# Performance work log

Hardware: AMD Instinct MI355X
Metric: run time of the kernel (lower is better)

The kernel has to match this reference:

```python
import jax, jax.numpy as jnp
import numpy as np

B, N, S, NS = 16, 4096, 512, 32
RADIUS = 0.4
EPS = 1e-5
CHANS = [6, 64, 64, 128]


def setup_inputs() -> dict:
    key = jax.random.key(0)
    ks = jax.random.split(key, 8)
    inp = {
        "xyz": jax.random.normal(ks[0], (B, 3, N), jnp.float32),
        "points": jax.random.normal(ks[1], (B, 3, N), jnp.float32),
    }
    for i in range(3):
        cin, cout = CHANS[i], CHANS[i + 1]
        inp[f"w{i}"] = jax.random.normal(ks[2 + i], (cout, cin), jnp.float32) * (1.0 / np.sqrt(cin))
        inp[f"b{i}"] = jnp.zeros((cout,), jnp.float32)
        inp[f"g{i}"] = jnp.ones((cout,), jnp.float32)
        inp[f"beta{i}"] = jnp.zeros((cout,), jnp.float32)
    return inp


def _fps(xyz):
    # xyz: [B, N, 3] -> indices [B, S] (deterministic start at index 0)
    n = xyz.shape[1]

    def step(carry, _):
        dist, far = carry
        centroid = jnp.take_along_axis(xyz, far[:, None, None], axis=1)  # [B,1,3]
        d = jnp.sum((xyz - centroid) ** 2, -1)                           # [B,N]
        dist = jnp.minimum(dist, d)
        nxt = jnp.argmax(dist, axis=-1).astype(jnp.int32)
        return (dist, nxt), far

    init = (jnp.full((xyz.shape[0], n), 1e10, xyz.dtype), jnp.zeros((xyz.shape[0],), jnp.int32))
    _, idx = jax.lax.scan(step, init, None, length=S)
    return idx.T  # [B, S]


def _query_ball(xyz, new_xyz):
    # xyz: [B,N,3], new_xyz: [B,S,3] -> group indices [B,S,NS]
    n = xyz.shape[1]
    sqr = (jnp.sum(new_xyz ** 2, -1)[:, :, None]
           + jnp.sum(xyz ** 2, -1)[:, None, :]
           - 2.0 * jnp.einsum('bsc,bnc->bsn', new_xyz, xyz))  # [B,S,N]
    grp = jnp.where(sqr <= RADIUS ** 2, jnp.arange(n, dtype=jnp.int32)[None, None, :], n)
    grp = jnp.sort(grp, axis=-1)[:, :, :NS]
    first = grp[:, :, :1]
    return jnp.where(grp == n, first, grp)


_gather = jax.vmap(lambda p, i: p[i])  # p:[N,C], i:[S,NS] -> [S,NS,C]


def _forward(xyz, points, params):
    xyz_t = jnp.transpose(xyz, (0, 2, 1))      # [B,N,3]
    pts_t = jnp.transpose(points, (0, 2, 1))   # [B,N,D]
    fps_idx = _fps(xyz_t)                      # [B,S]
    new_xyz = jnp.take_along_axis(xyz_t, fps_idx[:, :, None], axis=1)  # [B,S,3]
    grp = _query_ball(xyz_t, new_xyz)          # [B,S,NS]
    grouped_xyz = _gather(xyz_t, grp) - new_xyz[:, :, None, :]         # [B,S,NS,3]
    grouped_pts = _gather(pts_t, grp)          # [B,S,NS,D]
    feat = jnp.concatenate([grouped_xyz, grouped_pts], axis=-1)        # [B,S,NS,3+D]
    x = jnp.transpose(feat, (0, 3, 2, 1))      # [B,C,NS,S]
    for (w, b, g, beta) in params:
        x = jnp.einsum('oc,bcns->bons', w, x) + b[None, :, None, None]
        mean = jnp.mean(x, axis=(0, 2, 3), keepdims=True)
        var = jnp.mean((x - mean) ** 2, axis=(0, 2, 3), keepdims=True)
        x = (x - mean) * jax.lax.rsqrt(var + EPS)
        x = jax.nn.relu(x * g[None, :, None, None] + beta[None, :, None, None])
    new_points = jnp.max(x, axis=2)            # [B, C_out, S]
    return jnp.transpose(new_xyz, (0, 2, 1)), new_points


def reference(xyz, points, w0, b0, g0, beta0, w1, b1, g1, beta1, w2, b2, g2, beta2):
    params = [(w0, b0, g0, beta0), (w1, b1, g1, beta1), (w2, b2, g2, beta2)]
    return _forward(xyz, points, params)
```

## Files before the change

kernel.cpp:

```cpp
#include <hip/hip_runtime.h>
#include <math.h>

#define BB 16
#define NN 4096
#define SS 512
#define KK 32
#define NPIX (BB*SS*KK)
#define NGRP (BB*SS)

static constexpr float R2F  = (float)0.16000000000000003;
static constexpr float EPSF = 1e-5f;

constexpr size_t OFF_NXYZ = 0;
constexpr size_t OFF_GRP  = 98304;
constexpr size_t OFF_P1   = 98304 + 1048576;
constexpr size_t OFF_P2   = OFF_P1 + 32768;
constexpr size_t OFF_P3   = OFF_P2 + 32768;
constexpr size_t OFF_MR1  = OFF_P3 + 65536;
constexpr size_t OFF_MR2  = OFF_MR1 + 512;
constexpr size_t OFF_MR3  = OFF_MR2 + 512;
constexpr size_t OFF_Z3   = 2*1024*1024;
constexpr size_t Z3SZ     = (size_t)NPIX*128*4;
constexpr size_t OFF_Z2   = OFF_Z3 + Z3SZ;
constexpr size_t Z2SZ     = (size_t)NPIX*64*4;
constexpr size_t NEED_Z3  = OFF_Z3 + Z3SZ;
constexpr size_t NEED_Z2  = OFF_Z2 + Z2SZ;

#define DPP_FMAX(v, ctrl) { int _t = __builtin_amdgcn_update_dpp(              \
      __float_as_int(v), __float_as_int(v), ctrl, 0xf, 0xf, false);            \
      v = fmaxf(v, __int_as_float(_t)); }
#define DPP_UMIN(v, ctrl) { unsigned _t = (unsigned)__builtin_amdgcn_update_dpp( \
      (int)(v), (int)(v), ctrl, 0xf, 0xf, false);                              \
      v = (v < _t ? v : _t); }

__global__ __launch_bounds__(512) void fps_kernel(const float* __restrict__ xyz,
        float* __restrict__ out0, float* __restrict__ nxyz){
  const int b = blockIdx.x;
  const float* xb = xyz + (size_t)b*3*NN;
  __shared__ float4 pt4[NN];
  __shared__ __align__(16) unsigned long long skey[2][8];
  __shared__ int hist[SS];
  const int t = threadIdx.x;
  const int lane = t & 63, wv = t >> 6;
  float rx[8], ry[8], rz[8], rd[8];
#pragma unroll
  for (int j=0;j<8;j++){
    int i = t + 512*j;
    float x = xb[i], y = xb[NN+i], z = xb[2*NN+i];
    rx[j]=x; ry[j]=y; rz[j]=z;
    pt4[i] = make_float4(x,y,z,0.0f);
    rd[j]=1e10f;
  }
  __syncthreads();
  int far = 0;
  for (int s=0;s<SS;s++){
    const int buf = s & 1;
    float4 c = pt4[far];
    if (t==0) hist[s] = far;
    float bv = -1.0f;
#pragma unroll
    for (int j=0;j<8;j++){
      float dx=__fsub_rn(rx[j],c.x), dy=__fsub_rn(ry[j],c.y), dz=__fsub_rn(rz[j],c.z);
      float d2=__fadd_rn(__fadd_rn(__fmul_rn(dx,dx),__fmul_rn(dy,dy)),__fmul_rn(dz,dz));
      float nd=fminf(rd[j],d2);
      rd[j]=nd;
      bv = fmaxf(bv, nd);
    }
    DPP_FMAX(bv,0x111); DPP_FMAX(bv,0x112); DPP_FMAX(bv,0x114);
    DPP_FMAX(bv,0x118); DPP_FMAX(bv,0x142); DPP_FMAX(bv,0x143);
    const float vmax = __int_as_float(__builtin_amdgcn_readlane(__float_as_int(bv), 63));
    unsigned cand = 0xFFFFFFFFu;
#pragma unroll
    for (int j=7;j>=0;j--) if (rd[j]==vmax) cand = (unsigned)(t+512*j);
    DPP_UMIN(cand,0x111); DPP_UMIN(cand,0x112); DPP_UMIN(cand,0x114);
    DPP_UMIN(cand,0x118); DPP_UMIN(cand,0x142); DPP_UMIN(cand,0x143);
    if (lane==63){
      skey[buf][wv] = ((unsigned long long)(unsigned)__float_as_int(vmax) << 32)
                    | (unsigned)(~cand);
    }
    __syncthreads();
    unsigned long long k0=skey[buf][0], k1=skey[buf][1], k2=skey[buf][2], k3=skey[buf][3];
    unsigned long long k4=skey[buf][4], k5=skey[buf][5], k6=skey[buf][6], k7=skey[buf][7];
    unsigned long long m01=(k0>k1)?k0:k1, m23=(k2>k3)?k2:k3;
    unsigned long long m45=(k4>k5)?k4:k5, m67=(k6>k7)?k6:k7;
    unsigned long long mA=(m01>m23)?m01:m23, mB=(m45>m67)?m45:m67;
    unsigned long long m =(mA>mB)?mA:mB;
    far = (int)(~(unsigned)(m & 0xFFFFFFFFull));
  }
  __syncthreads();
  {
    int idx = hist[t];
    float4 c = pt4[idx];
    int gid = b*SS + t;
    nxyz[gid*3+0]=c.x; nxyz[gid*3+1]=c.y; nxyz[gid*3+2]=c.z;
    out0[(b*3+0)*SS+t]=c.x; out0[(b*3+1)*SS+t]=c.y; out0[(b*3+2)*SS+t]=c.z;
  }
}

__global__ __launch_bounds__(256) void ball_kernel(const float* __restrict__ xyz,
        const float* __restrict__ nxyz, int* __restrict__ grp){
  const int gw   = (blockIdx.x*256 + threadIdx.x) >> 6;
  const int lane = threadIdx.x & 63;
  if (gw >= NGRP) return;
  const int b = gw / SS;
  const float* xb = xyz + (size_t)b*3*NN;
  const float nx=nxyz[gw*3+0], ny=nxyz[gw*3+1], nz=nxyz[gw*3+2];
  const float sn = __fadd_rn(__fadd_rn(__fmul_rn(nx,nx),__fmul_rn(ny,ny)),__fmul_rn(nz,nz));
  int cnt=0, first=-1;
  int* g = grp + (size_t)gw*KK;
  for (int c=0;c<NN/64 && cnt<KK;c++){
    int i=c*64+lane;
    float x=xb[i], y=xb[NN+i], z=xb[2*NN+i];
    float sxx=__fadd_rn(__fadd_rn(__fmul_rn(x,x),__fmul_rn(y,y)),__fmul_rn(z,z));
    float dot=__fadd_rn(__fadd_rn(__fmul_rn(nx,x),__fmul_rn(ny,y)),__fmul_rn(nz,z));
    float sqr=__fsub_rn(__fadd_rn(sn,sxx),__fmul_rn(2.0f,dot));
    bool m = (sqr <= R2F);
    unsigned long long mask = __ballot(m);
    if (m){
      int pos = cnt + __popcll(mask & ((1ull<<lane)-1ull));
      if (pos < KK) g[pos] = i;
    }
    if (first<0 && mask) first = c*64 + (__ffsll((long long)mask) - 1);
    cnt += __popcll(mask);
  }
  if (cnt < KK && lane >= cnt && lane < KK) g[lane] = first;
}

__global__ void finalize_kernel(const double* __restrict__ part, float* __restrict__ mr, int C){
  int o = threadIdx.x;
  if (o < C){
    double s1=0.0, s2=0.0;
    for (int k=0;k<32;k++){ s1 += part[o*32+k]; s2 += part[(C+o)*32+k]; }
    const double n = (double)NPIX;
    double mean = s1/n;
    double var  = s2/n - mean*mean;
    mr[2*o]   = (float)mean;
    mr[2*o+1] = (float)(1.0/sqrt(var + (double)EPSF));
  }
}

constexpr int XIN = 0;
constexpr int W0F = 408;
constexpr int B0F = 792;
constexpr int W1F = 856;
constexpr int B1F = 4952;
constexpr int XBF = 5016;
constexpr int SRF = 9368;
constexpr int W2F = 9624;
constexpr int B2F = 17816;
constexpr int SM_SMALL = 9624;
constexpr int SM_BIG   = 17944;

template<int STAGE, bool STZ3, bool Z2IO>
__global__ __launch_bounds__(256,2) void mlp_kernel(
    const float* __restrict__ xyz, const float* __restrict__ pts,
    const float* __restrict__ nxyz, const int* __restrict__ grp,
    const float* __restrict__ w0, const float* __restrict__ b0,
    const float* __restrict__ mr1, const float* __restrict__ g0, const float* __restrict__ be0,
    const float* __restrict__ w1, const float* __restrict__ b1,
    const float* __restrict__ mr2, const float* __restrict__ g1, const float* __restrict__ be1,
    const float* __restrict__ w2, const float* __restrict__ b2,
    const float* __restrict__ mr3, const float* __restrict__ g2, const float* __restrict__ be2,
    double* __restrict__ part, float* __restrict__ out1,
    float* __restrict__ z2w, float* __restrict__ z3w)
{
  __shared__ float sm[(STAGE>=3)? SM_BIG : SM_SMALL];
  const int t   = threadIdx.x;
  const int blk = blockIdx.x;
  const int tx  = t & 15, ty = t >> 4;
  const int p0  = blk*64;
  const int slot = blk & 31;
  constexpr bool SKIP12 = (STAGE==3 && Z2IO);

  sm[SRF + t] = 0.0f;

  if constexpr (!SKIP12){
    for (int i=t;i<384;i+=256){ int o=i/6, c=i-o*6; sm[W0F + c*64 + o] = w0[i]; }
    if (t<64) sm[B0F+t] = b0[t];
    if constexpr (STAGE>=2){
      for (int i=t;i<4096;i+=256){ int o=i&63, c=i>>6; sm[W1F + c*64 + o] = w1[o*64+c]; }
      if (t<64) sm[B1F+t] = b1[t];
    }
    for (int i=t;i<384;i+=256){
      int c=i>>6, px=i&63, p=p0+px, gid=p>>5, bb=p>>14;
      int idx = grp[p];
      float v;
      if (c<3) v = __fsub_rn(xyz[(size_t)bb*3*NN + c*NN + idx], nxyz[gid*3+c]);
      else     v = pts[(size_t)bb*3*NN + (c-3)*NN + idx];
      sm[XIN + c*68 + px] = v;
    }
  }
  if constexpr (STAGE>=3){
    for (int i=t;i<8192;i+=256){ int o=i&127, c=i>>7; sm[W2F + c*128 + o] = w2[o*64+c]; }
    if (t<128) sm[B2F+t] = b2[t];
  }
  __syncthreads();

  float z[4][4];
  if constexpr (SKIP12){
#pragma unroll
    for (int i=0;i<4;i++){
      float4 v = *(const float4*)&z2w[(size_t)(p0 + ty*4 + i)*64 + tx*4];
      z[i][0]=v.x; z[i][1]=v.y; z[i][2]=v.z; z[i][3]=v.w;
    }
  } else {
#pragma unroll
    for (int i=0;i<4;i++)
#pragma unroll
      for (int j=0;j<4;j++) z[i][j]=0.0f;
#pragma unroll
    for (int k=0;k<6;k++){
      float4 xv = *(const float4*)&sm[XIN + k*68 + ty*4];
      float4 wv = *(const float4*)&sm[W0F + k*64 + tx*4];
      const float xs[4]={xv.x,xv.y,xv.z,xv.w};
      const float wsv[4]={wv.x,wv.y,wv.z,wv.w};
#pragma unroll
      for (int i=0;i<4;i++)
#pragma unroll
        for (int j=0;j<4;j++) z[i][j] = fmaf(xs[i], wsv[j], z[i][j]);
    }
#pragma unroll
    for (int i=0;i<4;i++)
#pragma unroll
      for (int j=0;j<4;j++) z[i][j] = __fadd_rn(z[i][j], sm[B0F + tx*4 + j]);

    if constexpr (STAGE==1){
#pragma unroll
      for (int j=0;j<4;j++){
        float s1=0.0f, s2=0.0f;
#pragma unroll
        for (int i=0;i<4;i++){ s1 = __fadd_rn(s1, z[i][j]); s2 = fmaf(z[i][j], z[i][j], s2); }
        atomicAdd(&sm[SRF + (tx*4+j)*2    ], s1);
        atomicAdd(&sm[SRF + (tx*4+j)*2 + 1], s2);
      }
      __syncthreads();
      if (t<128){ int ch=t>>1, m=t&1;
        atomicAdd(part + (size_t)((m? 64+ch : ch)*32 + slot), (double)sm[SRF+t]);
      }
      return;
    }

#pragma unroll
    for (int j=0;j<4;j++){
      int ch = tx*4+j;
      float m=mr1[2*ch], r=mr1[2*ch+1], gg=g0[ch], bt=be0[ch];
      float4 o;
      o.x = fmaxf(fmaf(__fmul_rn(__fsub_rn(z[0][j],m),r), gg, bt), 0.0f);
      o.y = fmaxf(fmaf(__fmul_rn(__fsub_rn(z[1][j],m),r), gg, bt), 0.0f);
      o.z = fmaxf(fmaf(__fmul_rn(__fsub_rn(z[2][j],m),r), gg, bt), 0.0f);
      o.w = fmaxf(fmaf(__fmul_rn(__fsub_rn(z[3][j],m),r), gg, bt), 0.0f);
      *(float4*)&sm[XBF + ch*68 + ty*4] = o;
    }
    __syncthreads();

#pragma unroll
    for (int i=0;i<4;i++)
#pragma unroll
      for (int j=0;j<4;j++) z[i][j]=0.0f;
#pragma unroll 8
    for (int k=0;k<64;k++){
      float4 xv = *(const float4*)&sm[XBF + k*68 + ty*4];
      float4 wv = *(const float4*)&sm[W1F + k*64 + tx*4];
      const float xs[4]={xv.x,xv.y,xv.z,xv.w};
      const float wsv[4]={wv.x,wv.y,wv.z,wv.w};
#pragma unroll
      for (int i=0;i<4;i++)
#pragma unroll
        for (int j=0;j<4;j++) z[i][j] = fmaf(xs[i], wsv[j], z[i][j]);
    }
#pragma unroll
    for (int i=0;i<4;i++)
#pragma unroll
      for (int j=0;j<4;j++) z[i][j] = __fadd_rn(z[i][j], sm[B1F + tx*4 + j]);

    if constexpr (STAGE==2){
      if constexpr (Z2IO){
#pragma unroll
        for (int i=0;i<4;i++)
          *(float4*)&z2w[(size_t)(p0 + ty*4 + i)*64 + tx*4]
              = make_float4(z[i][0], z[i][1], z[i][2], z[i][3]);
      }
#pragma unroll
      for (int j=0;j<4;j++){
        float s1=0.0f, s2=0.0f;
#pragma unroll
        for (int i=0;i<4;i++){ s1 = __fadd_rn(s1, z[i][j]); s2 = fmaf(z[i][j], z[i][j], s2); }
        atomicAdd(&sm[SRF + (tx*4+j)*2    ], s1);
        atomicAdd(&sm[SRF + (tx*4+j)*2 + 1], s2);
      }
      __syncthreads();
      if (t<128){ int ch=t>>1, m=t&1;
        atomicAdd(part + (size_t)((m? 64+ch : ch)*32 + slot), (double)sm[SRF+t]);
      }
      return;
    }
  }

  if constexpr (STAGE>=3){
    __syncthreads();
#pragma unroll
    for (int j=0;j<4;j++){
      int ch = tx*4+j;
      float m=mr2[2*ch], r=mr2[2*ch+1], gg=g1[ch], bt=be1[ch];
      float4 o;
      o.x = fmaxf(fmaf(__fmul_rn(__fsub_rn(z[0][j],m),r), gg, bt), 0.0f);
      o.y = fmaxf(fmaf(__fmul_rn(__fsub_rn(z[1][j],m),r), gg, bt), 0.0f);
      o.z = fmaxf(fmaf(__fmul_rn(__fsub_rn(z[2][j],m),r), gg, bt), 0.0f);
      o.w = fmaxf(fmaf(__fmul_rn(__fsub_rn(z[3][j],m),r), gg, bt), 0.0f);
      *(float4*)&sm[XBF + ch*68 + ty*4] = o;
    }
    __syncthreads();

    float a3[4][8];
#pragma unroll
    for (int i=0;i<4;i++)
#pragma unroll
      for (int j=0;j<8;j++) a3[i][j]=0.0f;
#pragma unroll 4
    for (int k=0;k<64;k++){
      float4 xv  = *(const float4*)&sm[XBF + k*68  + ty*4];
      float4 wv0 = *(const float4*)&sm[W2F + k*128 + tx*4];
      float4 wv1 = *(const float4*)&sm[W2F + k*128 + 64 + tx*4];
      const float xs[4]={xv.x,xv.y,xv.z,xv.w};
      const float wsv[8]={wv0.x,wv0.y,wv0.z,wv0.w, wv1.x,wv1.y,wv1.z,wv1.w};
#pragma unroll
      for (int i=0;i<4;i++)
#pragma unroll
        for (int j=0;j<8;j++) a3[i][j] = fmaf(xs[i], wsv[j], a3[i][j]);
    }
#pragma unroll
    for (int i=0;i<4;i++)
#pragma unroll
      for (int j=0;j<8;j++){
        int ch = (j<4)? (tx*4+j) : (64+tx*4+(j-4));
        a3[i][j] = __fadd_rn(a3[i][j], sm[B2F + ch]);
      }

    if constexpr (STAGE==3){
      if constexpr (STZ3){
#pragma unroll
        for (int i=0;i<4;i++){
          size_t p = (size_t)(p0 + ty*4 + i)*128;
          *(float4*)&z3w[p + tx*4]      = make_float4(a3[i][0],a3[i][1],a3[i][2],a3[i][3]);
          *(float4*)&z3w[p + 64 + tx*4] = make_float4(a3[i][4],a3[i][5],a3[i][6],a3[i][7]);
        }
      }
#pragma unroll
      for (int j=0;j<8;j++){
        int ch = (j<4)? (tx*4+j) : (64+tx*4+(j-4));
        float s1=0.0f, s2=0.0f;
#pragma unroll
        for (int i=0;i<4;i++){ s1 = __fadd_rn(s1, a3[i][j]); s2 = fmaf(a3[i][j], a3[i][j], s2); }
        atomicAdd(&sm[SRF + ch*2    ], s1);
        atomicAdd(&sm[SRF + ch*2 + 1], s2);
      }
      __syncthreads();
      { int ch=t>>1, m=t&1;
        atomicAdd(part + (size_t)((m? 128+ch : ch)*32 + slot), (double)sm[SRF+t]);
      }
      return;
    }

    if constexpr (STAGE==4){
      const int grp_l = ty>>3;
      unsigned* omax = (unsigned*)sm;
#pragma unroll
      for (int j=0;j<8;j++){
        int ch = (j<4)? (tx*4+j) : (64+tx*4+(j-4));
        float m=mr3[2*ch], r=mr3[2*ch+1], gg=g2[ch], bt=be2[ch];
        float vmax=0.0f;
#pragma unroll
        for (int i=0;i<4;i++){
          float v = fmaxf(fmaf(__fmul_rn(__fsub_rn(a3[i][j],m),r), gg, bt), 0.0f);
          vmax = fmaxf(vmax, v);
        }
        atomicMax(&omax[SRF + grp_l*128 + ch], __float_as_uint(vmax));
      }
      __syncthreads();
      { int g = t>>7, o = t&127;
        int gid = blk*2 + g, bb = gid>>9, s = gid&511;
        out1[((size_t)(bb*128+o))*512 + s] = __uint_as_float(omax[SRF + t]);
      }
    }
  }
}

__global__ __launch_bounds__(256) void maxpool_kernel(const float* __restrict__ z3,
        const float* __restrict__ mr3, const float* __restrict__ g2,
        const float* __restrict__ be2, float* __restrict__ out1){
  const int t = threadIdx.x;
  const int g = blockIdx.x*2 + (t>>7);
  const int o = t & 127;
  const int bb = g >> 9, s = g & 511;
  const float* zp = z3 + (size_t)g*KK*128 + o;
  float m=mr3[2*o], r=mr3[2*o+1], gg=g2[o], bt=be2[o];
  float mx = 0.0f;
#pragma unroll 8
  for (int k=0;k<KK;k++){
    float v = fmaxf(fmaf(__fmul_rn(__fsub_rn(zp[(size_t)k*128],m),r), gg, bt), 0.0f);
    mx = fmaxf(mx, v);
  }
  out1[((size_t)(bb*128+o))*SS + s] = mx;
}

extern "C" void kernel_launch(void* const* d_in, const int* in_sizes, int n_in,
                              void* d_out, int out_size, void* d_ws, size_t ws_size,
                              hipStream_t stream){
  const float* xyz = (const float*)d_in[0];
  const float* pts = (const float*)d_in[1];
  const float* w0  = (const float*)d_in[2];  const float* b0  = (const float*)d_in[3];
  const float* g0  = (const float*)d_in[4];  const float* be0 = (const float*)d_in[5];
  const float* w1  = (const float*)d_in[6];  const float* b1  = (const float*)d_in[7];
  const float* g1  = (const float*)d_in[8];  const float* be1 = (const float*)d_in[9];
  const float* w2  = (const float*)d_in[10]; const float* b2  = (const float*)d_in[11];
  const float* g2  = (const float*)d_in[12]; const float* be2 = (const float*)d_in[13];

  float* out  = (float*)d_out;
  float* out1 = out + BB*3*SS;
  char*  ws   = (char*)d_ws;

  float*  nxyz = (float*)(ws + OFF_NXYZ);
  int*    grp  = (int*)  (ws + OFF_GRP);
  double* p1   = (double*)(ws + OFF_P1);
  double* p2   = (double*)(ws + OFF_P2);
  double* p3   = (double*)(ws + OFF_P3);
  float*  mr1  = (float*)(ws + OFF_MR1);
  float*  mr2  = (float*)(ws + OFF_MR2);
  float*  mr3  = (float*)(ws + OFF_MR3);
  float*  z3w  = (float*)(ws + OFF_Z3);
  float*  z2w  = (float*)(ws + OFF_Z2);

  const bool stz3 = (ws_size >= NEED_Z3);
  const bool stz2 = (ws_size >= NEED_Z2);

  hipMemsetAsync(ws + OFF_P1, 0, 32768+32768+65536, stream);

  fps_kernel <<<BB, 512, 0, stream>>>(xyz, out, nxyz);
  ball_kernel<<<NGRP*64/256, 256, 0, stream>>>(xyz, nxyz, grp);

#define MLP_ARGS xyz, pts, nxyz, grp, w0, b0, mr1, g0, be0, w1, b1, mr2, g1, be1, w2, b2, mr3, g2, be2
  mlp_kernel<1,false,false><<<NPIX/64, 256, 0, stream>>>(MLP_ARGS, p1, out1, z2w, z3w);
  finalize_kernel<<<1,128,0,stream>>>(p1, mr1, 64);
  if (stz2) mlp_kernel<2,false,true ><<<NPIX/64, 256, 0, stream>>>(MLP_ARGS, p2, out1, z2w, z3w);
  else      mlp_kernel<2,false,false><<<NPIX/64, 256, 0, stream>>>(MLP_ARGS, p2, out1, z2w, z3w);
  finalize_kernel<<<1,128,0,stream>>>(p2, mr2, 64);
  if (stz2)      mlp_kernel<3,true ,true ><<<NPIX/64, 256, 0, stream>>>(MLP_ARGS, p3, out1, z2w, z3w);
  else if (stz3) mlp_kernel<3,true ,false><<<NPIX/64, 256, 0, stream>>>(MLP_ARGS, p3, out1, z2w, z3w);
  else           mlp_kernel<3,false,false><<<NPIX/64, 256, 0, stream>>>(MLP_ARGS, p3, out1, z2w, z3w);
  finalize_kernel<<<1,128,0,stream>>>(p3, mr3, 128);
  if (stz3) maxpool_kernel<<<NGRP/2, 256, 0, stream>>>(z3w, mr3, g2, be2, out1);
  else      mlp_kernel<4,false,false><<<NPIX/64, 256, 0, stream>>>(MLP_ARGS, p3, out1, z2w, z3w);
#undef MLP_ARGS
}
```

Before: 798.7 us.

## Interleave two batches per FPS block and fold workspace zeroing into FPS

The farthest-point-sampling kernel now runs two independent batch chains inside one 512-thread block, with 8 blocks instead of 16. Interleaving the distance updates, DPP reductions and shared-memory key merges of the two chains lets them share each per-step barrier and gives the serial, latency-bound loop more independent work to overlap. The separate memset of the statistics accumulators is removed, and the FPS kernel zeroes that buffer itself. In exchange each block uses about 128KB of LDS and twice the registers, and fewer blocks occupy the GPU.

```diff
diff --git a/kernel.cpp b/kernel.cpp
--- a/kernel.cpp
+++ b/kernel.cpp
@@ -34,66 +34,98 @@
       v = (v < _t ? v : _t); }
 
 __global__ __launch_bounds__(512) void fps_kernel(const float* __restrict__ xyz,
-        float* __restrict__ out0, float* __restrict__ nxyz){
-  const int b = blockIdx.x;
-  const float* xb = xyz + (size_t)b*3*NN;
-  __shared__ float4 pt4[NN];
-  __shared__ __align__(16) unsigned long long skey[2][8];
-  __shared__ int hist[SS];
-  const int t = threadIdx.x;
+        float* __restrict__ out0, float* __restrict__ nxyz, double* __restrict__ pzero){
+  const int t  = threadIdx.x;
+  const int bA = blockIdx.x*2, bB = bA+1;
+  const float* xA = xyz + (size_t)bA*3*NN;
+  const float* xB = xyz + (size_t)bB*3*NN;
+  __shared__ float4 ptA[NN];
+  __shared__ float4 ptB[NN];
+  __shared__ __align__(16) unsigned long long skA[2][8], skB[2][8];
+  __shared__ int hA[SS], hB[SS];
+  for (int i = blockIdx.x*512 + t; i < 16384; i += 8*512) pzero[i] = 0.0;
   const int lane = t & 63, wv = t >> 6;
-  float rx[8], ry[8], rz[8], rd[8];
+  float rxA[8],ryA[8],rzA[8],rdA[8], rxB[8],ryB[8],rzB[8],rdB[8];
 #pragma unroll
   for (int j=0;j<8;j++){
     int i = t + 512*j;
-    float x = xb[i], y = xb[NN+i], z = xb[2*NN+i];
-    rx[j]=x; ry[j]=y; rz[j]=z;
-    pt4[i] = make_float4(x,y,z,0.0f);
-    rd[j]=1e10f;
+    float x=xA[i], y=xA[NN+i], z=xA[2*NN+i];
+    rxA[j]=x; ryA[j]=y; rzA[j]=z; ptA[i]=make_float4(x,y,z,0.0f); rdA[j]=1e10f;
+    x=xB[i]; y=xB[NN+i]; z=xB[2*NN+i];
+    rxB[j]=x; ryB[j]=y; rzB[j]=z; ptB[i]=make_float4(x,y,z,0.0f); rdB[j]=1e10f;
   }
   __syncthreads();
-  int far = 0;
+  int farA = 0, farB = 0;
   for (int s=0;s<SS;s++){
     const int buf = s & 1;
-    float4 c = pt4[far];
-    if (t==0) hist[s] = far;
-    float bv = -1.0f;
+    float4 cA = ptA[farA];
+    float4 cB = ptB[farB];
+    if (t==0){ hA[s]=farA; hB[s]=farB; }
+    float bvA = -1.0f, bvB = -1.0f;
 #pragma unroll
     for (int j=0;j<8;j++){
-      float dx=__fsub_rn(rx[j],c.x), dy=__fsub_rn(ry[j],c.y), dz=__fsub_rn(rz[j],c.z);
+      float dx=__fsub_rn(rxA[j],cA.x), dy=__fsub_rn(ryA[j],cA.y), dz=__fsub_rn(rzA[j],cA.z);
       float d2=__fadd_rn(__fadd_rn(__fmul_rn(dx,dx),__fmul_rn(dy,dy)),__fmul_rn(dz,dz));
-      float nd=fminf(rd[j],d2);
-      rd[j]=nd;
-      bv = fmaxf(bv, nd);
-    }
-    DPP_FMAX(bv,0x111); DPP_FMAX(bv,0x112); DPP_FMAX(bv,0x114);
-    DPP_FMAX(bv,0x118); DPP_FMAX(bv,0x142); DPP_FMAX(bv,0x143);
-    const float vmax = __int_as_float(__builtin_amdgcn_readlane(__float_as_int(bv), 63));
-    unsigned cand = 0xFFFFFFFFu;
-#pragma unroll
-    for (int j=7;j>=0;j--) if (rd[j]==vmax) cand = (unsigned)(t+512*j);
-    DPP_UMIN(cand,0x111); DPP_UMIN(cand,0x112); DPP_UMIN(cand,0x114);
-    DPP_UMIN(cand,0x118); DPP_UMIN(cand,0x142); DPP_UMIN(cand,0x143);
+      float nd=fminf(rdA[j],d2); rdA[j]=nd; bvA=fmaxf(bvA,nd);
+      dx=__fsub_rn(rxB[j],cB.x); dy=__fsub_rn(ryB[j],cB.y); dz=__fsub_rn(rzB[j],cB.z);
+      d2=__fadd_rn(__fadd_rn(__fmul_rn(dx,dx),__fmul_rn(dy,dy)),__fmul_rn(dz,dz));
+      nd=fminf(rdB[j],d2); rdB[j]=nd; bvB=fmaxf(bvB,nd);
+    }
+    DPP_FMAX(bvA,0x111); DPP_FMAX(bvB,0x111);
+    DPP_FMAX(bvA,0x112); DPP_FMAX(bvB,0x112);
+    DPP_FMAX(bvA,0x114); DPP_FMAX(bvB,0x114);
+    DPP_FMAX(bvA,0x118); DPP_FMAX(bvB,0x118);
+    DPP_FMAX(bvA,0x142); DPP_FMAX(bvB,0x142);
+    DPP_FMAX(bvA,0x143); DPP_FMAX(bvB,0x143);
+    const float vmA = __int_as_float(__builtin_amdgcn_readlane(__float_as_int(bvA), 63));
+    const float vmB = __int_as_float(__builtin_amdgcn_readlane(__float_as_int(bvB), 63));
+    unsigned cnA = 0xFFFFFFFFu, cnB = 0xFFFFFFFFu;
+#pragma unroll
+    for (int j=7;j>=0;j--){
+      if (rdA[j]==vmA) cnA = (unsigned)(t+512*j);
+      if (rdB[j]==vmB) cnB = (unsigned)(t+512*j);
+    }
+    DPP_UMIN(cnA,0x111); DPP_UMIN(cnB,0x111);
+    DPP_UMIN(cnA,0x112); DPP_UMIN(cnB,0x112);
+    DPP_UMIN(cnA,0x114); DPP_UMIN(cnB,0x114);
+    DPP_UMIN(cnA,0x118); DPP_UMIN(cnB,0x118);
+    DPP_UMIN(cnA,0x142); DPP_UMIN(cnB,0x142);
+    DPP_UMIN(cnA,0x143); DPP_UMIN(cnB,0x143);
     if (lane==63){
-      skey[buf][wv] = ((unsigned long long)(unsigned)__float_as_int(vmax) << 32)
-                    | (unsigned)(~cand);
+      skA[buf][wv] = ((unsigned long long)(unsigned)__float_as_int(vmA) << 32)
+                   | (unsigned)(~cnA);
+      skB[buf][wv] = ((unsigned long long)(unsigned)__float_as_int(vmB) << 32)
+                   | (unsigned)(~cnB);
     }
     __syncthreads();
-    unsigned long long k0=skey[buf][0], k1=skey[buf][1], k2=skey[buf][2], k3=skey[buf][3];
-    unsigned long long k4=skey[buf][4], k5=skey[buf][5], k6=skey[buf][6], k7=skey[buf][7];
-    unsigned long long m01=(k0>k1)?k0:k1, m23=(k2>k3)?k2:k3;
-    unsigned long long m45=(k4>k5)?k4:k5, m67=(k6>k7)?k6:k7;
-    unsigned long long mA=(m01>m23)?m01:m23, mB=(m45>m67)?m45:m67;
-    unsigned long long m =(mA>mB)?mA:mB;
-    far = (int)(~(unsigned)(m & 0xFFFFFFFFull));
+    {
+      unsigned long long k0=skA[buf][0],k1=skA[buf][1],k2=skA[buf][2],k3=skA[buf][3];
+      unsigned long long k4=skA[buf][4],k5=skA[buf][5],k6=skA[buf][6],k7=skA[buf][7];
+      unsigned long long p0=skB[buf][0],p1=skB[buf][1],p2=skB[buf][2],p3=skB[buf][3];
+      unsigned long long p4=skB[buf][4],p5=skB[buf][5],p6=skB[buf][6],p7=skB[buf][7];
+      unsigned long long a01=(k0>k1)?k0:k1, a23=(k2>k3)?k2:k3;
+      unsigned long long a45=(k4>k5)?k4:k5, a67=(k6>k7)?k6:k7;
+      unsigned long long b01=(p0>p1)?p0:p1, b23=(p2>p3)?p2:p3;
+      unsigned long long b45=(p4>p5)?p4:p5, b67=(p6>p7)?p6:p7;
+      unsigned long long aA=(a01>a23)?a01:a23, aB=(a45>a67)?a45:a67;
+      unsigned long long bA2=(b01>b23)?b01:b23, bB2=(b45>b67)?b45:b67;
+      unsigned long long mA=(aA>aB)?aA:aB, mB=(bA2>bB2)?bA2:bB2;
+      farA = (int)(~(unsigned)(mA & 0xFFFFFFFFull));
+      farB = (int)(~(unsigned)(mB & 0xFFFFFFFFull));
+    }
   }
   __syncthreads();
   {
-    int idx = hist[t];
-    float4 c = pt4[idx];
-    int gid = b*SS + t;
+    int idx = hA[t];
+    float4 c = ptA[idx];
+    int gid = bA*SS + t;
     nxyz[gid*3+0]=c.x; nxyz[gid*3+1]=c.y; nxyz[gid*3+2]=c.z;
-    out0[(b*3+0)*SS+t]=c.x; out0[(b*3+1)*SS+t]=c.y; out0[(b*3+2)*SS+t]=c.z;
+    out0[(bA*3+0)*SS+t]=c.x; out0[(bA*3+1)*SS+t]=c.y; out0[(bA*3+2)*SS+t]=c.z;
+    idx = hB[t];
+    c = ptB[idx];
+    gid = bB*SS + t;
+    nxyz[gid*3+0]=c.x; nxyz[gid*3+1]=c.y; nxyz[gid*3+2]=c.z;
+    out0[(bB*3+0)*SS+t]=c.x; out0[(bB*3+1)*SS+t]=c.y; out0[(bB*3+2)*SS+t]=c.z;
   }
 }
 
@@ -433,9 +465,7 @@
   const bool stz3 = (ws_size >= NEED_Z3);
   const bool stz2 = (ws_size >= NEED_Z2);
 
-  hipMemsetAsync(ws + OFF_P1, 0, 32768+32768+65536, stream);
-
-  fps_kernel <<<BB, 512, 0, stream>>>(xyz, out, nxyz);
+  fps_kernel <<<BB/2, 512, 0, stream>>>(xyz, out, nxyz, p1);
   ball_kernel<<<NGRP*64/256, 256, 0, stream>>>(xyz, nxyz, grp);
 
 #define MLP_ARGS xyz, pts, nxyz, grp, w0, b0, mr1, g0, be0, w1, b1, mr2, g1, be1, w2, b2, mr3, g2, be2
```

After: 1.070 ms. 1.34x slower.
